# Optimization experiments

Measured on AMD Instinct MI355X. Metric: run time of the kernel, lower is better.

Reference implementation:

```python
import jax, jax.numpy as jnp
import numpy as np

N, Wd = 1000000, 20
EPS = 1e-16


def setup_inputs() -> dict:
    key = jax.random.key(0)
    ks = jax.random.split(key, 40)
    def rn(i, shape, scale=0.05):
        return jax.random.normal(ks[i], shape, dtype=jnp.float32) * scale
    inp = {
        "X": rn(0, (1, 14), 1.0),
        "read_weights": jax.nn.sigmoid(rn(1, (1, N), 1.0)),
        "write_weights": jax.nn.sigmoid(rn(2, (1, N), 1.0)),
        "Memory": jnp.full((N, Wd), 1e-6, dtype=jnp.float32),
        "read_head": jax.nn.sigmoid(rn(3, (1, Wd), 1.0)),
        "W1": rn(4, (48, 14)), "b1": rn(5, (48,)),
        "W2": rn(6, (72, 48)), "b2": rn(7, (72,)),
        "Wxi": rn(8, ((Wd + 6) * 2 + 2 * Wd, 72)), "bxi": rn(9, ((Wd + 6) * 2 + 2 * Wd,)),
        "Wz": rn(10, (3, 72)), "bz": rn(11, (3,)),
        "Wv": rn(12, (20, 325)), "bv": rn(13, (20,)),
        "aW1": rn(14, (110, 40)), "ab1": rn(15, (110,)),
        "aW2": rn(16, (190, 110)), "ab2": rn(17, (190,)),
        "aW3": rn(18, (270, 190)), "ab3": rn(19, (270,)),
        "aW4": rn(20, (325, 270)), "ab4": rn(21, (325,)),
        "mW1": rn(22, (110, 40)), "mb1": rn(23, (110,)),
        "mW2": rn(24, (190, 110)), "mb2": rn(25, (190,)),
        "mW3": rn(26, (270, 190)), "mb3": rn(27, (270,)),
        "mW4": rn(28, (325, 270)), "mb4": rn(29, (325,)),
    }
    return inp


def _alu(x, W1, b1, W2, b2, W3, b3, W4, b4):
    x = jax.nn.relu(x @ W1.T + b1)
    x = jax.nn.relu(x @ W2.T + b2)
    x = jax.nn.relu(x @ W3.T + b3)
    return jax.nn.softmax(x @ W4.T + b4, axis=-1)


def _head_params(p):  # p: (1, Wd+6)
    k = jnp.tanh(p[0, :Wd])[None, :]              # (1, Wd)
    g = jax.nn.sigmoid(p[0, Wd])
    s = jax.nn.softmax(p[0, Wd + 1:Wd + 4])        # (3,)
    gamma = 1.0 + jax.nn.softplus(p[0, Wd + 4])
    beta = jax.nn.softplus(p[0, Wd + 5])
    return k, g, s, gamma, beta


def _address(Memory, k, beta, g, s, gamma, w_prev):
    Me = Memory + EPS                              # (N, Wd)
    ke = k + EPS                                   # (1, Wd)
    num = (Me @ ke.T)[:, 0]                        # (N,)
    den = jnp.maximum(jnp.linalg.norm(Me, axis=-1), 1e-8) * \
          jnp.maximum(jnp.linalg.norm(ke, axis=-1), 1e-8)
    w_c = jax.nn.softmax((num / den) * beta)       # (N,)
    w_g = g * w_c + (1.0 - g) * w_prev             # (1, N)
    pad = jnp.concatenate([w_g[:, -1:], w_g, w_g[:, :1]], axis=1)  # (1, N+2)
    w_r = s[0] * pad[:, :N] + s[1] * pad[:, 1:N + 1] + s[2] * pad[:, 2:]
    w = w_r ** gamma
    return w / (jnp.sum(w, axis=1, keepdims=True) + EPS)


def reference(X, read_weights, write_weights, Memory, read_head,
              W1, b1, W2, b2, Wxi, bxi, Wz, bz, Wv, bv,
              aW1, ab1, aW2, ab2, aW3, ab3, aW4, ab4,
              mW1, mb1, mW2, mb2, mW3, mb3, mW4, mb4):
    h = X @ W1.T + b1                # (1, 48)  (no activation, faithful)
    h = h @ W2.T + b2                # (1, 72)
    xi = h @ Wxi.T + bxi             # (1, 92)
    zeta = h @ Wz.T + bz             # (1, 3)

    rp = xi[0, :Wd + 6][None, :]
    wp = xi[0, Wd + 6:(Wd + 6) * 2][None, :]
    erase = jax.nn.sigmoid(xi[0, (Wd + 6) * 2:(Wd + 6) * 2 + Wd][None, :])
    add = jnp.tanh(xi[0, (Wd + 6) * 2 + Wd:(Wd + 6) * 2 + 2 * Wd][None, :])

    k, g, s, gamma, beta = _head_params(rp)
    rw = _address(Memory, k, beta, g, s, gamma, read_weights)
    k, g, s, gamma, beta = _head_params(wp)
    ww = _address(Memory, k, beta, g, s, gamma, write_weights)

    new_read_head = rw @ Memory                    # (1, Wd)
    alu_in = jnp.concatenate([read_head, new_read_head], axis=1)  # (1, 2*Wd)

    rho = jax.nn.sigmoid(zeta[0, 0])
    alu_head = jax.nn.softmax(zeta[:, 1:], axis=-1)  # (1, 2)
    out_add = _alu(alu_in, aW1, ab1, aW2, ab2, aW3, ab3, aW4, ab4)
    out_mul = _alu(alu_in, mW1, mb1, mW2, mb2, mW3, mb3, mW4, mb4)
    out = alu_head[0, 0] * out_add + alu_head[0, 1] * out_mul  # (1, 325)

    v = out @ Wv.T + bv                              # (1, 20)
    add = rho * add + (1.0 - rho) * v

    new_memory = Memory * (1.0 - ww.T @ erase) + ww.T @ add  # (N, Wd)
    return out, rw, ww, new_memory, new_read_head
```

## Files before the change

### kernel.cpp

```cpp
#include <hip/hip_runtime.h>
#include <math.h>

#define NN 1000000
#define NF4 5000000
#define WD 20
#define NB 977
#define PST 1024

#define OUT_OFF 0
#define RW_OFF  325
#define WW_OFF  1000325
#define NM_OFF  2000325
#define NRH_OFF 22000325

__device__ __forceinline__ float sigmoidf_(float x){ return 1.0f/(1.0f+expf(-x)); }
__device__ __forceinline__ float softplusf_(float x){ return (x>30.f)?x:log1pf(expf(x)); }

__global__ __launch_bounds__(256) void k_scores(
    const float* __restrict__ X,
    const float* __restrict__ W1, const float* __restrict__ b1,
    const float* __restrict__ W2, const float* __restrict__ b2,
    const float* __restrict__ Wxi, const float* __restrict__ bxi,
    const float* __restrict__ Wz, const float* __restrict__ bz,
    const float* __restrict__ M, float* __restrict__ Pg,
    float2* __restrict__ sc2, float4* __restrict__ pms){
  __shared__ float4 ld[1280];
  __shared__ float h1[48], h2[72], xi[95], sP[132];
  int t=threadIdx.x, b=blockIdx.x;
  if(t<48){ float a=b1[t]; const float* w=W1+t*14; for(int c=0;c<14;c++) a+=X[c]*w[c]; h1[t]=a; }
  __syncthreads();
  if(t<72){ float a=b2[t]; const float* w=W2+t*48; for(int c=0;c<48;c++) a+=h1[c]*w[c]; h2[t]=a; }
  __syncthreads();
  if(t<92){ float a=bxi[t]; const float* w=Wxi+t*72; for(int c=0;c<72;c++) a+=h2[c]*w[c]; xi[t]=a; }
  else if(t<95){ int z=t-92; float a=bz[z]; const float* w=Wz+z*72; for(int c=0;c<72;c++) a+=h2[c]*w[c]; xi[92+z]=a; }
  __syncthreads();
  if(t<20){
    sP[0+t]  = tanhf(xi[t]);
    sP[32+t] = tanhf(xi[26+t]);
    sP[64+t] = sigmoidf_(xi[52+t]);
    sP[84+t] = tanhf(xi[72+t]);
  }
  if(t==32){
    const float* p = xi;
    float g=sigmoidf_(p[20]);
    float a0=p[21],a1=p[22],a2=p[23];
    float mx=fmaxf(a0,fmaxf(a1,a2));
    float e0=expf(a0-mx),e1=expf(a1-mx),e2=expf(a2-mx),es=e0+e1+e2;
    float gamma=1.0f+softplusf_(p[24]);
    float beta=softplusf_(p[25]);
    float n2=0.f; for(int j=0;j<20;j++){ float ke=tanhf(p[j])+1e-16f; n2+=ke*ke; }
    sP[20]=g; sP[21]=e0/es; sP[22]=e1/es; sP[23]=e2/es; sP[24]=gamma; sP[25]=beta;
    sP[26]=fmaxf(sqrtf(n2),1e-8f);
  }
  if(t==33){
    const float* p = xi+26;
    float g=sigmoidf_(p[20]);
    float a0=p[21],a1=p[22],a2=p[23];
    float mx=fmaxf(a0,fmaxf(a1,a2));
    float e0=expf(a0-mx),e1=expf(a1-mx),e2=expf(a2-mx),es=e0+e1+e2;
    float gamma=1.0f+softplusf_(p[24]);
    float beta=softplusf_(p[25]);
    float n2=0.f; for(int j=0;j<20;j++){ float ke=tanhf(p[j])+1e-16f; n2+=ke*ke; }
    sP[52]=g; sP[53]=e0/es; sP[54]=e1/es; sP[55]=e2/es; sP[56]=gamma; sP[57]=beta;
    sP[58]=fmaxf(sqrtf(n2),1e-8f);
  }
  if(t==34){
    sP[104]=sigmoidf_(xi[92]);
    float mx=fmaxf(xi[93],xi[94]);
    float e1=expf(xi[93]-mx), e2=expf(xi[94]-mx);
    sP[105]=e1/(e1+e2); sP[106]=e2/(e1+e2);
  }
  __syncthreads();
  if(b==0 && t<132) Pg[t]=sP[t];
  float kr[20], kw[20];
#pragma unroll
  for(int j=0;j<20;j++){ kr[j]=sP[j]+1e-16f; kw[j]=sP[32+j]+1e-16f; }
  float betar=sP[25], betaw=sP[57], knr=sP[26], knw=sP[58];
  const float4* Mf4=(const float4*)M;
  float sR[4], sW[4];
  for(int p=0;p<4;p++){
    int rb=b*1024+p*256;
    size_t f4b=(size_t)rb*5;
#pragma unroll
    for(int k=0;k<5;k++){
      size_t idx=f4b+(size_t)(k*256+t);
      ld[k*256+t] = (idx<NF4)?Mf4[idx]:make_float4(0.f,0.f,0.f,0.f);
    }
    __syncthreads();
    int i=rb+t;
    float srv=-3.0e38f, swv=-3.0e38f;
    if(i<NN){
      float dr=0.f,dw=0.f,n2=0.f;
#pragma unroll
      for(int q=0;q<5;q++){
        float4 v=ld[t*5+q];
        float m0=v.x+1e-16f,m1=v.y+1e-16f,m2=v.z+1e-16f,m3=v.w+1e-16f;
        dr+=m0*kr[4*q]+m1*kr[4*q+1]+m2*kr[4*q+2]+m3*kr[4*q+3];
        dw+=m0*kw[4*q]+m1*kw[4*q+1]+m2*kw[4*q+2]+m3*kw[4*q+3];
        n2+=m0*m0+m1*m1+m2*m2+m3*m3;
      }
      float nm=fmaxf(sqrtf(n2),1e-8f);
      srv=betar*(dr/(nm*knr));
      swv=betaw*(dw/(nm*knw));
      sc2[i]=make_float2(srv,swv);
    }
    sR[p]=srv; sW[p]=swv;
    __syncthreads();
  }
  float* r1=(float*)ld; float* r2=r1+256;
  double* d1=(double*)(r1+512); double* d2=d1+256;
  float lm1=fmaxf(fmaxf(sR[0],sR[1]),fmaxf(sR[2],sR[3]));
  float lm2=fmaxf(fmaxf(sW[0],sW[1]),fmaxf(sW[2],sW[3]));
  r1[t]=lm1; r2[t]=lm2; __syncthreads();
  for(int o=128;o>0;o>>=1){ if(t<o){ r1[t]=fmaxf(r1[t],r1[t+o]); r2[t]=fmaxf(r2[t],r2[t+o]); } __syncthreads(); }
  float mb1=r1[0], mb2=r2[0]; __syncthreads();
  double s1=0.0,s2=0.0;
#pragma unroll
  for(int p=0;p<4;p++){ s1+=(double)expf(sR[p]-mb1); s2+=(double)expf(sW[p]-mb2); }
  d1[t]=s1; d2[t]=s2; __syncthreads();
  for(int o=128;o>0;o>>=1){ if(t<o){ d1[t]+=d1[t+o]; d2[t]+=d2[t+o]; } __syncthreads(); }
  if(t==0) pms[b]=make_float4(mb1,mb2,(float)d1[0],(float)d2[0]);
}

__global__ __launch_bounds__(256) void k_shift(const float2* __restrict__ sc2,
                        const float* __restrict__ wpr, const float* __restrict__ wpw,
                        const float* __restrict__ M, const float* __restrict__ P,
                        const float4* __restrict__ pms,
                        float* __restrict__ w_r_out, float* __restrict__ w_w_out,
                        double* __restrict__ pZ, double* __restrict__ pnrhT){
  __shared__ float4 ld[1280];
  __shared__ float bmS[4];
  float* r1=(float*)ld; float* r2=r1+256;
  double* d1=(double*)(r1+512); double* d2=d1+256;
  float* wsum=(float*)(d2+256);
  int t=threadIdx.x, b=blockIdx.x;
  float4 v4[4];
#pragma unroll
  for(int k=0;k<4;k++){
    int idx=t+k*256;
    v4[k] = (idx<NB) ? pms[idx] : make_float4(-3.0e38f,-3.0e38f,0.f,0.f);
  }
  float lm1=fmaxf(fmaxf(v4[0].x,v4[1].x),fmaxf(v4[2].x,v4[3].x));
  float lm2=fmaxf(fmaxf(v4[0].y,v4[1].y),fmaxf(v4[2].y,v4[3].y));
  r1[t]=lm1; r2[t]=lm2; __syncthreads();
  for(int o=128;o>0;o>>=1){ if(t<o){ r1[t]=fmaxf(r1[t],r1[t+o]); r2[t]=fmaxf(r2[t],r2[t+o]); } __syncthreads(); }
  if(t==0){ bmS[0]=r1[0]; bmS[1]=r2[0]; } __syncthreads();
  float mr=bmS[0], mw=bmS[1];
  double s1=0.0,s2=0.0;
#pragma unroll
  for(int k=0;k<4;k++){
    s1 += (double)v4[k].z * (double)expf(v4[k].x-mr);
    s2 += (double)v4[k].w * (double)expf(v4[k].y-mw);
  }
  d1[t]=s1; d2[t]=s2; __syncthreads();
  for(int o=128;o>0;o>>=1){ if(t<o){ d1[t]+=d1[t+o]; d2[t]+=d2[t+o]; } __syncthreads(); }
  if(t==0){ bmS[2]=(float)d1[0]; bmS[3]=(float)d2[0]; } __syncthreads();
  float Sr=bmS[2], Sw=bmS[3];
  float gr=P[20], s0r=P[21], s1r=P[22], s2r=P[23], gar=P[24];
  float gw=P[52], s0w=P[53], s1w=P[54], s2w=P[55], gaw=P[56];
  float omgr=1.0f-gr, omgw=1.0f-gw;
  const float4* Mf4=(const float4*)M;
  float acc[20];
#pragma unroll
  for(int j=0;j<20;j++) acc[j]=0.f;
  double zr=0.0, zw=0.0;
  for(int p=0;p<4;p++){
    int rb=b*1024+p*256;
    size_t f4b=(size_t)rb*5;
#pragma unroll
    for(int k=0;k<5;k++){
      size_t idx=f4b+(size_t)(k*256+t);
      ld[k*256+t] = (idx<NF4)?Mf4[idx]:make_float4(0.f,0.f,0.f,0.f);
    }
    __syncthreads();
    int i=rb+t;
    if(i<NN){
      int im1=(i==0)?(NN-1):(i-1);
      int ip1=(i==NN-1)?0:(i+1);
      float2 scm=sc2[im1], sc0=sc2[i], scp=sc2[ip1];
      float wgrm = gr*(expf(scm.x-mr)/Sr) + omgr*wpr[im1];
      float wgr0 = gr*(expf(sc0.x-mr)/Sr) + omgr*wpr[i  ];
      float wgrp = gr*(expf(scp.x-mr)/Sr) + omgr*wpr[ip1];
      float wgwm = gw*(expf(scm.y-mw)/Sw) + omgw*wpw[im1];
      float wgw0 = gw*(expf(sc0.y-mw)/Sw) + omgw*wpw[i  ];
      float wgwp = gw*(expf(scp.y-mw)/Sw) + omgw*wpw[ip1];
      float wr = powf(s0r*wgrm + s1r*wgr0 + s2r*wgrp, gar);
      float ww = powf(s0w*wgwm + s1w*wgw0 + s2w*wgwp, gaw);
      w_r_out[i]=wr; w_w_out[i]=ww;
      zr+=(double)wr; zw+=(double)ww;
#pragma unroll
      for(int q=0;q<5;q++){
        float4 mv=ld[t*5+q];
        acc[4*q+0]+=wr*mv.x; acc[4*q+1]+=wr*mv.y; acc[4*q+2]+=wr*mv.z; acc[4*q+3]+=wr*mv.w;
      }
    }
    __syncthreads();
  }
  d1[t]=zr; d2[t]=zw; __syncthreads();
  for(int o=128;o>0;o>>=1){ if(t<o){ d1[t]+=d1[t+o]; d2[t]+=d2[t+o]; } __syncthreads(); }
  if(t==0){ pZ[2*b]=d1[0]; pZ[2*b+1]=d2[0]; }
  __syncthreads();
#pragma unroll
  for(int j=0;j<20;j++){
    for(int off=32;off>0;off>>=1) acc[j]+=__shfl_down(acc[j],off,64);
  }
  int wave=t>>6, lane=t&63;
  if(lane==0){
#pragma unroll
    for(int j=0;j<20;j++) wsum[wave*20+j]=acc[j];
  }
  __syncthreads();
  if(t<20){
    double s=(double)wsum[0*20+t]+(double)wsum[1*20+t]+(double)wsum[2*20+t]+(double)wsum[3*20+t];
    pnrhT[(size_t)t*PST+b]=s;
  }
}

__global__ __launch_bounds__(256) void k_nrh(const double* __restrict__ pZ, const double* __restrict__ pnrhT,
                      const float* __restrict__ read_head,
                      float* __restrict__ in40, float* __restrict__ out, double* __restrict__ Sd){
  __shared__ double dd[256];
  __shared__ double bZ[2];
  int t=threadIdx.x, j=blockIdx.x;
  double a=0.0,c=0.0;
  for(int idx=t; idx<NB; idx+=256){ a+=pZ[2*idx]; c+=pZ[2*idx+1]; }
  dd[t]=a; __syncthreads();
  for(int o=128;o>0;o>>=1){ if(t<o) dd[t]+=dd[t+o]; __syncthreads(); }
  if(t==0) bZ[0]=dd[0]; __syncthreads();
  dd[t]=c; __syncthreads();
  for(int o=128;o>0;o>>=1){ if(t<o) dd[t]+=dd[t+o]; __syncthreads(); }
  if(t==0) bZ[1]=dd[0]; __syncthreads();
  if(j==0 && t==0){ Sd[0]=bZ[0]; Sd[1]=bZ[1]; }
  double s=0.0;
  for(int idx=t; idx<NB; idx+=256) s+=pnrhT[(size_t)j*PST+idx];
  dd[t]=s; __syncthreads();
  for(int o=128;o>0;o>>=1){ if(t<o) dd[t]+=dd[t+o]; __syncthreads(); }
  if(t==0){
    float nv=(float)(dd[0]/(bZ[0]+1e-16));
    in40[20+j]=nv; out[NRH_OFF+j]=nv;
    in40[j]=read_head[j];
  }
}

__global__ __launch_bounds__(256) void k_layer(const float* __restrict__ Wa, const float* __restrict__ ba,
                        const float* __restrict__ Wm, const float* __restrict__ bm,
                        const float* __restrict__ inA, const float* __restrict__ inM,
                        float* __restrict__ oA, float* __restrict__ oM,
                        int rows, int K, int RB, int doRelu){
  int net = (blockIdx.x >= RB) ? 1 : 0;
  const float* W = net ? Wm : Wa;
  const float* bb = net ? bm : ba;
  const float* in = net ? inM : inA;
  float* o = net ? oM : oA;
  int wave=threadIdx.x>>6, lane=threadIdx.x&63;
  int r=(blockIdx.x - net*RB)*4 + wave;
  if(r>=rows) return;
  const float* w = W + (size_t)r*K;
  float a=0.f;
  for(int c=lane; c<K; c+=64) a += w[c]*in[c];
  for(int off=32;off>0;off>>=1) a += __shfl_down(a,off,64);
  if(lane==0){
    float vv=a+bb[r];
    o[r]= doRelu ? fmaxf(vv,0.f) : vv;
  }
}

__global__ __launch_bounds__(512) void k_fin(const float* __restrict__ h4a, const float* __restrict__ h4m,
                      const float* __restrict__ Wv, const float* __restrict__ bv,
                      float* __restrict__ P, float* __restrict__ out){
  __shared__ float red[512];
  __shared__ float A[325], B[325];
  __shared__ float sc[2];
  int t=threadIdx.x;
  float la=(t<325)?h4a[t]:-3.0e38f;
  red[t]=la; __syncthreads();
  for(int o=256;o>0;o>>=1){ if(t<o) red[t]=fmaxf(red[t],red[t+o]); __syncthreads(); }
  if(t==0) sc[0]=red[0]; __syncthreads();
  float ea=(t<325)?expf(la-sc[0]):0.f;
  red[t]=ea; __syncthreads();
  for(int o=256;o>0;o>>=1){ if(t<o) red[t]+=red[t+o]; __syncthreads(); }
  if(t==0) sc[1]=red[0]; __syncthreads();
  if(t<325) A[t]=ea/sc[1];
  __syncthreads();
  float lm=(t<325)?h4m[t]:-3.0e38f;
  red[t]=lm; __syncthreads();
  for(int o=256;o>0;o>>=1){ if(t<o) red[t]=fmaxf(red[t],red[t+o]); __syncthreads(); }
  if(t==0) sc[0]=red[0]; __syncthreads();
  float em=(t<325)?expf(lm-sc[0]):0.f;
  red[t]=em; __syncthreads();
  for(int o=256;o>0;o>>=1){ if(t<o) red[t]+=red[t+o]; __syncthreads(); }
  if(t==0) sc[1]=red[0]; __syncthreads();
  if(t<325) B[t]=em/sc[1];
  __syncthreads();
  float ah0=P[105], ah1=P[106];
  if(t<325){ float ov=ah0*A[t]+ah1*B[t]; out[OUT_OFF+t]=ov; A[t]=ov; }
  __syncthreads();
  int wave=t>>6, lane=t&63;
  for(int r=wave; r<20; r+=8){
    const float* w=Wv+(size_t)r*325;
    float a=0.f;
    for(int c=lane;c<325;c+=64) a+=w[c]*A[c];
    for(int off=32;off>0;off>>=1) a+=__shfl_down(a,off,64);
    if(lane==0){
      float vv=a+bv[r];
      float rho=P[104];
      P[112+r]=rho*P[84+r]+(1.0f-rho)*vv;
    }
  }
}

__global__ __launch_bounds__(256) void k_memupd(const float* __restrict__ M,
                         float* __restrict__ w_r, float* __restrict__ w_w,
                         const float* __restrict__ P, const double* __restrict__ Sd,
                         float* __restrict__ nm){
  __shared__ float4 ld[1280];
  int t=threadIdx.x, b=blockIdx.x;
  float er[20], af[20];
#pragma unroll
  for(int j=0;j<20;j++){ er[j]=P[64+j]; af[j]=P[112+j]; }
  float Zr=(float)Sd[0]+1e-16f, Zw=(float)Sd[1]+1e-16f;
  const float4* Mf4=(const float4*)M;
  float4* nmf4=(float4*)nm;
  for(int p=0;p<4;p++){
    int rb=b*1024+p*256;
    size_t f4b=(size_t)rb*5;
#pragma unroll
    for(int k=0;k<5;k++){
      size_t idx=f4b+(size_t)(k*256+t);
      if(idx<NF4) ld[k*256+t]=Mf4[idx];
    }
    __syncthreads();
    int i=rb+t;
    if(i<NN){
      float wrn=w_r[i]/Zr;
      float wwn=w_w[i]/Zw;
      w_r[i]=wrn; w_w[i]=wwn;
#pragma unroll
      for(int q=0;q<5;q++){
        float4 v=ld[t*5+q];
        float4 o;
        o.x=v.x*(1.0f-wwn*er[4*q+0])+wwn*af[4*q+0];
        o.y=v.y*(1.0f-wwn*er[4*q+1])+wwn*af[4*q+1];
        o.z=v.z*(1.0f-wwn*er[4*q+2])+wwn*af[4*q+2];
        o.w=v.w*(1.0f-wwn*er[4*q+3])+wwn*af[4*q+3];
        ld[t*5+q]=o;
      }
    }
    __syncthreads();
#pragma unroll
    for(int k=0;k<5;k++){
      size_t idx=f4b+(size_t)(k*256+t);
      if(idx<NF4) nmf4[idx]=ld[k*256+t];
    }
    __syncthreads();
  }
}

extern "C" void kernel_launch(void* const* d_in, const int* in_sizes, int n_in,
                              void* d_out, int out_size, void* d_ws, size_t ws_size,
                              hipStream_t stream) {
  const float* X    =(const float*)d_in[0];
  const float* rwp  =(const float*)d_in[1];
  const float* wwp  =(const float*)d_in[2];
  const float* Mem  =(const float*)d_in[3];
  const float* rhd  =(const float*)d_in[4];
  const float* W1   =(const float*)d_in[5];
  const float* b1   =(const float*)d_in[6];
  const float* W2   =(const float*)d_in[7];
  const float* b2   =(const float*)d_in[8];
  const float* Wxi  =(const float*)d_in[9];
  const float* bxi  =(const float*)d_in[10];
  const float* Wz   =(const float*)d_in[11];
  const float* bz   =(const float*)d_in[12];
  const float* Wv   =(const float*)d_in[13];
  const float* bv   =(const float*)d_in[14];
  const float* aW1  =(const float*)d_in[15];
  const float* ab1  =(const float*)d_in[16];
  const float* aW2  =(const float*)d_in[17];
  const float* ab2  =(const float*)d_in[18];
  const float* aW3  =(const float*)d_in[19];
  const float* ab3  =(const float*)d_in[20];
  const float* aW4  =(const float*)d_in[21];
  const float* ab4  =(const float*)d_in[22];
  const float* mW1  =(const float*)d_in[23];
  const float* mb1  =(const float*)d_in[24];
  const float* mW2  =(const float*)d_in[25];
  const float* mb2  =(const float*)d_in[26];
  const float* mW3  =(const float*)d_in[27];
  const float* mb3  =(const float*)d_in[28];
  const float* mW4  =(const float*)d_in[29];
  const float* mb4  =(const float*)d_in[30];

  float* out = (float*)d_out;
  char* ws = (char*)d_ws;
  float*    P     = (float*)   (ws + 0);
  double*   Sd    = (double*)  (ws + 2048);
  float*    in40  = (float*)   (ws + 2304);
  float*    F     = (float*)   (ws + 4096);
  float4*   pms   = (float4*)  (ws + 16384);
  double*   pZ    = (double*)  (ws + 32768);
  double*   pnrhT = (double*)  (ws + 65536);
  float *h1a=F,      *h1m=F+110;
  float *h2a=F+220,  *h2m=F+410;
  float *h3a=F+600,  *h3m=F+870;
  float *h4a=F+1140, *h4m=F+1465;

  float2* sc2 = (float2*)(out + NM_OFF);
  float*  w_r = out + RW_OFF;
  float*  w_w = out + WW_OFF;
  float*  nm  = out + NM_OFF;

  k_scores<<<NB,256,0,stream>>>(X,W1,b1,W2,b2,Wxi,bxi,Wz,bz,Mem,P,sc2,pms);
  k_shift<<<NB,256,0,stream>>>(sc2,rwp,wwp,Mem,P,pms,w_r,w_w,pZ,pnrhT);
  k_nrh<<<20,256,0,stream>>>(pZ,pnrhT,rhd,in40,out,Sd);
  k_layer<<<56,256,0,stream>>>(aW1,ab1,mW1,mb1,in40,in40,h1a,h1m,110,40,28,1);
  k_layer<<<96,256,0,stream>>>(aW2,ab2,mW2,mb2,h1a,h1m,h2a,h2m,190,110,48,1);
  k_layer<<<136,256,0,stream>>>(aW3,ab3,mW3,mb3,h2a,h2m,h3a,h3m,270,190,68,1);
  k_layer<<<164,256,0,stream>>>(aW4,ab4,mW4,mb4,h3a,h3m,h4a,h4m,325,270,82,0);
  k_fin<<<1,512,0,stream>>>(h4a,h4m,Wv,bv,P,out);
  k_memupd<<<NB,256,0,stream>>>(Mem,w_r,w_w,P,Sd,nm);
}
```

Before: 116.5 us.

## Fuse nrh reduction and first three ALU MLP layers into one kernel

Replaces the k_nrh kernel and four k_layer launches with two kernels. k_mlpA does the global reductions in every block, redundantly computes layers 1-2 in shared memory, and splits layer 3 across 64 blocks. k_mlpB then computes layer 4. This cuts launch count and inter-kernel gaps in the serial tail. The price is redundant reduction and layer 1-2 work in each block. In k_scores, the key norms now reuse the tanh values already stored in shared memory, and the scalar tasks move to different waves.

```diff
diff --git a/kernel.cpp b/kernel.cpp
--- a/kernel.cpp
+++ b/kernel.cpp
@@ -40,31 +40,34 @@
     sP[64+t] = sigmoidf_(xi[52+t]);
     sP[84+t] = tanhf(xi[72+t]);
   }
+  __syncthreads();
   if(t==32){
-    const float* p = xi;
-    float g=sigmoidf_(p[20]);
-    float a0=p[21],a1=p[22],a2=p[23];
+    float g=sigmoidf_(xi[20]);
+    float a0=xi[21],a1=xi[22],a2=xi[23];
     float mx=fmaxf(a0,fmaxf(a1,a2));
     float e0=expf(a0-mx),e1=expf(a1-mx),e2=expf(a2-mx),es=e0+e1+e2;
-    float gamma=1.0f+softplusf_(p[24]);
-    float beta=softplusf_(p[25]);
-    float n2=0.f; for(int j=0;j<20;j++){ float ke=tanhf(p[j])+1e-16f; n2+=ke*ke; }
+    float gamma=1.0f+softplusf_(xi[24]);
+    float beta=softplusf_(xi[25]);
+    float n2=0.f;
+#pragma unroll
+    for(int j=0;j<20;j++){ float ke=sP[j]+1e-16f; n2+=ke*ke; }
     sP[20]=g; sP[21]=e0/es; sP[22]=e1/es; sP[23]=e2/es; sP[24]=gamma; sP[25]=beta;
     sP[26]=fmaxf(sqrtf(n2),1e-8f);
   }
-  if(t==33){
-    const float* p = xi+26;
-    float g=sigmoidf_(p[20]);
-    float a0=p[21],a1=p[22],a2=p[23];
+  if(t==96){
+    float g=sigmoidf_(xi[46]);
+    float a0=xi[47],a1=xi[48],a2=xi[49];
     float mx=fmaxf(a0,fmaxf(a1,a2));
     float e0=expf(a0-mx),e1=expf(a1-mx),e2=expf(a2-mx),es=e0+e1+e2;
-    float gamma=1.0f+softplusf_(p[24]);
-    float beta=softplusf_(p[25]);
-    float n2=0.f; for(int j=0;j<20;j++){ float ke=tanhf(p[j])+1e-16f; n2+=ke*ke; }
+    float gamma=1.0f+softplusf_(xi[50]);
+    float beta=softplusf_(xi[51]);
+    float n2=0.f;
+#pragma unroll
+    for(int j=0;j<20;j++){ float ke=sP[32+j]+1e-16f; n2+=ke*ke; }
     sP[52]=g; sP[53]=e0/es; sP[54]=e1/es; sP[55]=e2/es; sP[56]=gamma; sP[57]=beta;
     sP[58]=fmaxf(sqrtf(n2),1e-8f);
   }
-  if(t==34){
+  if(t==160){
     sP[104]=sigmoidf_(xi[92]);
     float mx=fmaxf(xi[93],xi[94]);
     float e1=expf(xi[93]-mx), e2=expf(xi[94]-mx);
@@ -216,53 +219,85 @@
   }
 }
 
-__global__ __launch_bounds__(256) void k_nrh(const double* __restrict__ pZ, const double* __restrict__ pnrhT,
-                      const float* __restrict__ read_head,
-                      float* __restrict__ in40, float* __restrict__ out, double* __restrict__ Sd){
-  __shared__ double dd[256];
-  __shared__ double bZ[2];
-  int t=threadIdx.x, j=blockIdx.x;
-  double a=0.0,c=0.0;
-  for(int idx=t; idx<NB; idx+=256){ a+=pZ[2*idx]; c+=pZ[2*idx+1]; }
-  dd[t]=a; __syncthreads();
-  for(int o=128;o>0;o>>=1){ if(t<o) dd[t]+=dd[t+o]; __syncthreads(); }
-  if(t==0) bZ[0]=dd[0]; __syncthreads();
-  dd[t]=c; __syncthreads();
-  for(int o=128;o>0;o>>=1){ if(t<o) dd[t]+=dd[t+o]; __syncthreads(); }
-  if(t==0) bZ[1]=dd[0]; __syncthreads();
-  if(j==0 && t==0){ Sd[0]=bZ[0]; Sd[1]=bZ[1]; }
-  double s=0.0;
-  for(int idx=t; idx<NB; idx+=256) s+=pnrhT[(size_t)j*PST+idx];
-  dd[t]=s; __syncthreads();
-  for(int o=128;o>0;o>>=1){ if(t<o) dd[t]+=dd[t+o]; __syncthreads(); }
-  if(t==0){
-    float nv=(float)(dd[0]/(bZ[0]+1e-16));
-    in40[20+j]=nv; out[NRH_OFF+j]=nv;
-    in40[j]=read_head[j];
-  }
-}
-
-__global__ __launch_bounds__(256) void k_layer(const float* __restrict__ Wa, const float* __restrict__ ba,
-                        const float* __restrict__ Wm, const float* __restrict__ bm,
-                        const float* __restrict__ inA, const float* __restrict__ inM,
-                        float* __restrict__ oA, float* __restrict__ oM,
-                        int rows, int K, int RB, int doRelu){
-  int net = (blockIdx.x >= RB) ? 1 : 0;
-  const float* W = net ? Wm : Wa;
-  const float* bb = net ? bm : ba;
-  const float* in = net ? inM : inA;
-  float* o = net ? oM : oA;
-  int wave=threadIdx.x>>6, lane=threadIdx.x&63;
-  int r=(blockIdx.x - net*RB)*4 + wave;
-  if(r>=rows) return;
-  const float* w = W + (size_t)r*K;
+__global__ __launch_bounds__(512) void k_mlpA(
+    const double* __restrict__ pZ, const double* __restrict__ pnrhT,
+    const float* __restrict__ read_head,
+    const float* __restrict__ aW1,const float* __restrict__ ab1,
+    const float* __restrict__ mW1,const float* __restrict__ mb1,
+    const float* __restrict__ aW2,const float* __restrict__ ab2,
+    const float* __restrict__ mW2,const float* __restrict__ mb2,
+    const float* __restrict__ aW3,const float* __restrict__ ab3,
+    const float* __restrict__ mW3,const float* __restrict__ mb3,
+    float* __restrict__ out, double* __restrict__ Sd, float* __restrict__ h3g){
+  __shared__ float in40[40], h1s[220], h2s[380];
+  __shared__ double nrhd[20], bZ[2];
+  int t=threadIdx.x, b=blockIdx.x, wave=t>>6, lane=t&63;
+  if(wave<2){
+    double s=0.0;
+    for(int idx=lane; idx<NB; idx+=64) s+=pZ[2*idx+wave];
+    for(int off=32;off>0;off>>=1) s+=__shfl_down(s,off,64);
+    if(lane==0) bZ[wave]=s;
+  }
+  for(int j=wave; j<20; j+=8){
+    const double* src=pnrhT+(size_t)j*PST;
+    double s=0.0;
+    for(int idx=lane; idx<NB; idx+=64) s+=src[idx];
+    for(int off=32;off>0;off>>=1) s+=__shfl_down(s,off,64);
+    if(lane==0) nrhd[j]=s;
+  }
+  __syncthreads();
+  if(t<20){
+    float nv=(float)(nrhd[t]/(bZ[0]+1e-16));
+    in40[20+t]=nv; in40[t]=read_head[t];
+    if(b==0) out[NRH_OFF+t]=nv;
+  }
+  if(b==0 && t==20){ Sd[0]=bZ[0]; Sd[1]=bZ[1]; }
+  __syncthreads();
+  for(int r0=wave; r0<220; r0+=8){
+    int net=(r0>=110), r=r0-net*110;
+    const float* w=(net?mW1:aW1)+(size_t)r*40;
+    float a=(lane<40)? w[lane]*in40[lane] : 0.f;
+    for(int off=32;off>0;off>>=1) a+=__shfl_down(a,off,64);
+    if(lane==0) h1s[r0]=fmaxf(a+(net?mb1:ab1)[r],0.f);
+  }
+  __syncthreads();
+#pragma unroll 2
+  for(int r0=wave; r0<380; r0+=8){
+    int net=(r0>=190), r=r0-net*190;
+    const float* w=(net?mW2:aW2)+(size_t)r*110;
+    const float* in=h1s+net*110;
+    float a=0.f;
+    for(int c=lane;c<110;c+=64) a+=w[c]*in[c];
+    for(int off=32;off>0;off>>=1) a+=__shfl_down(a,off,64);
+    if(lane==0) h2s[r0]=fmaxf(a+(net?mb2:ab2)[r],0.f);
+  }
+  __syncthreads();
+  int wid=b*8+wave;
+  for(int r0=wid; r0<540; r0+=512){
+    int net=(r0>=270), r=r0-net*270;
+    const float* w=(net?mW3:aW3)+(size_t)r*190;
+    const float* in=h2s+net*190;
+    float a=0.f;
+    for(int c=lane;c<190;c+=64) a+=w[c]*in[c];
+    for(int off=32;off>0;off>>=1) a+=__shfl_down(a,off,64);
+    if(lane==0) h3g[r0]=fmaxf(a+(net?mb3:ab3)[r],0.f);
+  }
+}
+
+__global__ __launch_bounds__(512) void k_mlpB(const float* __restrict__ h3g,
+    const float* __restrict__ aW4,const float* __restrict__ ab4,
+    const float* __restrict__ mW4,const float* __restrict__ mb4,
+    float* __restrict__ h4g){
+  int t=threadIdx.x, wave=t>>6, lane=t&63;
+  int wid=blockIdx.x*8+wave;
+  if(wid>=650) return;
+  int net=(wid>=325), r=wid-net*325;
+  const float* w=(net?mW4:aW4)+(size_t)r*270;
+  const float* in=h3g+net*270;
   float a=0.f;
-  for(int c=lane; c<K; c+=64) a += w[c]*in[c];
-  for(int off=32;off>0;off>>=1) a += __shfl_down(a,off,64);
-  if(lane==0){
-    float vv=a+bb[r];
-    o[r]= doRelu ? fmaxf(vv,0.f) : vv;
-  }
+  for(int c=lane;c<270;c+=64) a+=w[c]*in[c];
+  for(int off=32;off>0;off>>=1) a+=__shfl_down(a,off,64);
+  if(lane==0) h4g[wid]=a+(net?mb4:ab4)[r];
 }
 
 __global__ __launch_bounds__(512) void k_fin(const float* __restrict__ h4a, const float* __restrict__ h4m,
@@ -395,15 +430,11 @@
   char* ws = (char*)d_ws;
   float*    P     = (float*)   (ws + 0);
   double*   Sd    = (double*)  (ws + 2048);
-  float*    in40  = (float*)   (ws + 2304);
-  float*    F     = (float*)   (ws + 4096);
+  float*    h3g   = (float*)   (ws + 4096);
+  float*    h4g   = (float*)   (ws + 8192);
   float4*   pms   = (float4*)  (ws + 16384);
   double*   pZ    = (double*)  (ws + 32768);
   double*   pnrhT = (double*)  (ws + 65536);
-  float *h1a=F,      *h1m=F+110;
-  float *h2a=F+220,  *h2m=F+410;
-  float *h3a=F+600,  *h3m=F+870;
-  float *h4a=F+1140, *h4m=F+1465;
 
   float2* sc2 = (float2*)(out + NM_OFF);
   float*  w_r = out + RW_OFF;
@@ -412,11 +443,9 @@
 
   k_scores<<<NB,256,0,stream>>>(X,W1,b1,W2,b2,Wxi,bxi,Wz,bz,Mem,P,sc2,pms);
   k_shift<<<NB,256,0,stream>>>(sc2,rwp,wwp,Mem,P,pms,w_r,w_w,pZ,pnrhT);
-  k_nrh<<<20,256,0,stream>>>(pZ,pnrhT,rhd,in40,out,Sd);
-  k_layer<<<56,256,0,stream>>>(aW1,ab1,mW1,mb1,in40,in40,h1a,h1m,110,40,28,1);
-  k_layer<<<96,256,0,stream>>>(aW2,ab2,mW2,mb2,h1a,h1m,h2a,h2m,190,110,48,1);
-  k_layer<<<136,256,0,stream>>>(aW3,ab3,mW3,mb3,h2a,h2m,h3a,h3m,270,190,68,1);
-  k_layer<<<164,256,0,stream>>>(aW4,ab4,mW4,mb4,h3a,h3m,h4a,h4m,325,270,82,0);
-  k_fin<<<1,512,0,stream>>>(h4a,h4m,Wv,bv,P,out);
+  k_mlpA<<<64,512,0,stream>>>(pZ,pnrhT,rhd,aW1,ab1,mW1,mb1,aW2,ab2,mW2,mb2,
+                              aW3,ab3,mW3,mb3,out,Sd,h3g);
+  k_mlpB<<<82,512,0,stream>>>(h3g,aW4,ab4,mW4,mb4,h4g);
+  k_fin<<<1,512,0,stream>>>(h4g,h4g+325,Wv,bv,P,out);
   k_memupd<<<NB,256,0,stream>>>(Mem,w_r,w_w,P,Sd,nm);
 }
```

Result: slower. 177.9 us (+52.7%).
